# Optimization experiments

Hardware: AMD Instinct MI355X
Metric: run time of the kernel (lower is better)

Reference implementation:

```python
import jax, jax.numpy as jnp
import numpy as np

N = 50000          # nodes
E = 1250000        # edges (no self loops in raw data)
H = 2              # heads
C = 32             # out channels per head
DIN = 64           # dim_node
ED = 16            # edge_dim
G = 16             # graphs in batch
NC = 5             # num classes
SLOPE = 0.2        # GATConv leaky_relu negative_slope


def _glorot(key, shape):
    fan = shape[0] if len(shape) == 2 else shape[-1]
    return jax.random.normal(key, shape, jnp.float32) * (1.0 / np.sqrt(fan))


def setup_inputs() -> dict:
    key = jax.random.key(0)
    ks = jax.random.split(key, 24)
    x = jax.random.normal(ks[0], (N, DIN), jnp.float32)
    dst = jax.random.randint(ks[1], (E,), 0, N)
    off = jax.random.randint(ks[2], (E,), 1, N)
    src = (dst + off) % N  # guarantees src != dst (PyG removes self loops before re-adding)
    edge_index = jnp.stack([src, dst]).astype(jnp.int32)
    edge_attr = jax.random.normal(ks[3], (E, ED), jnp.float32)
    batch = jnp.sort(jax.random.randint(ks[4], (N,), 0, G)).astype(jnp.int32)
    inp = dict(x=x, edge_index=edge_index, edge_attr=edge_attr, batch=batch)
    # layer 1: in=DIN, heads=H, out=C, concat -> H*C
    inp["W1"] = _glorot(ks[5], (DIN, H * C)); inp["asrc1"] = _glorot(ks[6], (H, C))
    inp["adst1"] = _glorot(ks[7], (H, C)); inp["We1"] = _glorot(ks[8], (ED, H * C))
    inp["ae1"] = _glorot(ks[9], (H, C)); inp["b1"] = jnp.zeros((H * C,), jnp.float32)
    # layer 2: in=H*C, heads=H, out=C, concat
    inp["W2"] = _glorot(ks[10], (H * C, H * C)); inp["asrc2"] = _glorot(ks[11], (H, C))
    inp["adst2"] = _glorot(ks[12], (H, C)); inp["We2"] = _glorot(ks[13], (ED, H * C))
    inp["ae2"] = _glorot(ks[14], (H, C)); inp["b2"] = jnp.zeros((H * C,), jnp.float32)
    # layer 3: in=H*C, heads=1, out=C, concat=False
    inp["W3"] = _glorot(ks[15], (H * C, C)); inp["asrc3"] = _glorot(ks[16], (1, C))
    inp["adst3"] = _glorot(ks[17], (1, C)); inp["We3"] = _glorot(ks[18], (ED, C))
    inp["ae3"] = _glorot(ks[19], (1, C)); inp["b3"] = jnp.zeros((C,), jnp.float32)
    # ffn: Linear(C, NC) + softmax (dropout is identity in eval)
    inp["Wf"] = _glorot(ks[20], (C, NC)); inp["bf"] = jnp.zeros((NC,), jnp.float32)
    return inp


def _gat_layer(h_in, src, dst, eattr, W, asrc, adst, We, ae, b, heads, out, concat):
    n = h_in.shape[0]
    h = (h_in @ W).reshape(n, heads, out)                      # [N,H,C]
    s_src = jnp.einsum('nhc,hc->nh', h, asrc)                  # per-node src scores
    s_dst = jnp.einsum('nhc,hc->nh', h, adst)
    he = (eattr @ We).reshape(-1, heads, out)                  # [E,H,C]
    s_e = jnp.einsum('ehc,hc->eh', he, ae)
    logit = jax.nn.leaky_relu(s_src[src] + s_dst[dst] + s_e, SLOPE)  # [E,H]
    m = jax.ops.segment_max(logit, dst, num_segments=n)
    ex = jnp.exp(logit - m[dst])
    den = jax.ops.segment_sum(ex, dst, num_segments=n)
    alpha = ex / (den[dst] + 1e-16)                            # segment softmax per dst node
    agg = jax.ops.segment_sum(h[src] * alpha[..., None], dst, num_segments=n)  # [N,H,C]
    out_x = agg.reshape(n, heads * out) if concat else agg.mean(axis=1)
    return out_x + b


def _gat_forward(x, edge_index, edge_attr, batch,
                 W1, asrc1, adst1, We1, ae1, b1,
                 W2, asrc2, adst2, We2, ae2, b2,
                 W3, asrc3, adst3, We3, ae3, b3,
                 Wf, bf):
    src, dst = edge_index[0], edge_index[1]
    n = x.shape[0]
    # add_self_loops with fill_value='mean': self-loop edge_attr = mean of incoming edge_attr
    deg = jax.ops.segment_sum(jnp.ones((src.shape[0],), x.dtype), dst, num_segments=n)
    self_attr = jax.ops.segment_sum(edge_attr, dst, num_segments=n) / jnp.maximum(deg, 1.0)[:, None]
    loop = jnp.arange(n, dtype=src.dtype)
    src_a = jnp.concatenate([src, loop])
    dst_a = jnp.concatenate([dst, loop])
    eattr_a = jnp.concatenate([edge_attr, self_attr], axis=0)

    h = jax.nn.relu(_gat_layer(x, src_a, dst_a, eattr_a, W1, asrc1, adst1, We1, ae1, b1, H, C, True))
    h = jax.nn.relu(_gat_layer(h, src_a, dst_a, eattr_a, W2, asrc2, adst2, We2, ae2, b2, H, C, True))
    h = jax.nn.relu(_gat_layer(h, src_a, dst_a, eattr_a, W3, asrc3, adst3, We3, ae3, b3, 1, C, False))

    # global mean pool per graph
    cnt = jax.ops.segment_sum(jnp.ones((n,), h.dtype), batch, num_segments=G)
    pooled = jax.ops.segment_sum(h, batch, num_segments=G) / jnp.maximum(cnt, 1.0)[:, None]
    # ffn: Dropout (identity at eval) -> Linear -> Softmax(dim=1)
    return jax.nn.softmax(pooled @ Wf + bf, axis=1)


def reference(x, edge_index, edge_attr, batch,
              W1, asrc1, adst1, We1, ae1, b1,
              W2, asrc2, adst2, We2, ae2, b2,
              W3, asrc3, adst3, We3, ae3, b3,
              Wf, bf):
    return _gat_forward(x, edge_index, edge_attr, batch,
                        W1, asrc1, adst1, We1, ae1, b1,
                        W2, asrc2, adst2, We2, ae2, b2,
                        W3, asrc3, adst3, We3, ae3, b3,
                        Wf, bf)
```

## Files before the change

kernel.cpp:

```cpp
#include <hip/hip_runtime.h>
#include <math.h>

#define NN 50000
#define EE 1250000
#define GG 16
#define NCLS 5
#define NBIN 391
#define BINSHIFT 7
#define CAPB 3900

constexpr size_t AL(size_t x){ return (x + 255) & ~size_t(255); }
constexpr size_t OFF_DEG    = 0;
constexpr size_t OFF_ROWPTR = OFF_DEG + AL((size_t)NN*4);
constexpr size_t OFF_CURSOR = OFF_ROWPTR + AL((size_t)(NN+1)*4);
constexpr size_t OFF_SRCS   = OFF_CURSOR + AL((size_t)NN*4);
constexpr size_t OFF_SE12   = OFF_SRCS + AL((size_t)EE*2);
constexpr size_t OFF_SE34   = OFF_SE12 + AL((size_t)EE*4);
constexpr size_t OFF_SE5    = OFF_SE34 + AL((size_t)EE*4);
constexpr size_t OFF_SSRC   = OFF_SE5 + AL((size_t)EE*2);
constexpr size_t OFF_SDST   = OFF_SSRC + AL((size_t)NN*2*4);
constexpr size_t OFF_STAG   = OFF_SDST + AL((size_t)NN*2*4);
constexpr size_t OFF_BUFH   = OFF_STAG + AL((size_t)NBIN*CAPB*16);
constexpr size_t OFF_BUFO   = OFF_BUFH + AL((size_t)NN*32*4);
constexpr size_t OFF_WEFF   = OFF_BUFO + AL((size_t)NN*64*4);
constexpr size_t OFF_POOL   = OFF_WEFF + AL(80*4);

__device__ __forceinline__ float leaky(float x){ return x > 0.f ? x : 0.2f*x; }
__device__ __forceinline__ unsigned rne_bf16(float x){
    unsigned u = __float_as_uint(x);
    return (u + 0x7FFFu + ((u >> 16) & 1u)) >> 16;
}

__global__ void weff_kernel(const float* __restrict__ We1, const float* __restrict__ ae1,
                            const float* __restrict__ We2, const float* __restrict__ ae2,
                            const float* __restrict__ We3, const float* __restrict__ ae3,
                            float* __restrict__ weff){
    int t = threadIdx.x;
    if (t >= 80) return;
    int j = t >> 4, d = t & 15;
    const float* We; const float* ae; int hc, h;
    if (j == 0){ We = We1; ae = ae1; hc = 64; h = 0; }
    else if (j == 1){ We = We1; ae = ae1; hc = 64; h = 1; }
    else if (j == 2){ We = We2; ae = ae2; hc = 64; h = 0; }
    else if (j == 3){ We = We2; ae = ae2; hc = 64; h = 1; }
    else { We = We3; ae = ae3; hc = 32; h = 0; }
    float s = 0.f;
    for (int c = 0; c < 32; ++c) s += We[d*hc + h*32 + c] * ae[h*32 + c];
    weff[j*16 + d] = s;
}

__global__ void binit_kernel(int* __restrict__ bincursor){
    int b = blockIdx.x*256 + threadIdx.x;
    if (b < NBIN) bincursor[b] = b*CAPB;
}

__global__ void binA_kernel(const int* __restrict__ src, const int* __restrict__ dst,
                            const float* __restrict__ eattr, const float* __restrict__ weff,
                            int* __restrict__ bincursor, int4* __restrict__ staging, int nE){
    __shared__ int lcount[NBIN];
    __shared__ int lbase[NBIN];
    __shared__ float w[80];
    int tid = threadIdx.x;
    if (tid < 80) w[tid] = weff[tid];
    for (int i = tid; i < NBIN; i += 1024) lcount[i] = 0;
    __syncthreads();
    int base = blockIdx.x * 8192;
    int w0[8], bn[8], idx[8]; unsigned p01[8], p23[8], p4[8];
    #pragma unroll
    for (int k = 0; k < 8; ++k){
        int i = base + k*1024 + tid;
        if (i < nE){
            int d = dst[i];
            int s = src[i];
            bn[k]  = d >> BINSHIFT;
            w0[k]  = s | ((d & 127) << 16);
            const float4* row = (const float4*)(eattr + (size_t)i*16);
            float4 a0 = row[0], a1 = row[1], a2 = row[2], a3 = row[3];
            float a[16] = {a0.x,a0.y,a0.z,a0.w, a1.x,a1.y,a1.z,a1.w,
                           a2.x,a2.y,a2.z,a2.w, a3.x,a3.y,a3.z,a3.w};
            float sj[5];
            #pragma unroll
            for (int j = 0; j < 5; ++j){
                float s2 = 0.f;
                #pragma unroll
                for (int d2 = 0; d2 < 16; ++d2) s2 += a[d2]*w[j*16+d2];
                sj[j] = s2;
            }
            p01[k] = rne_bf16(sj[0]) | (rne_bf16(sj[1]) << 16);
            p23[k] = rne_bf16(sj[2]) | (rne_bf16(sj[3]) << 16);
            p4[k]  = rne_bf16(sj[4]);
            idx[k] = atomicAdd(&lcount[bn[k]], 1);
        } else bn[k] = -1;
    }
    __syncthreads();
    for (int i = tid; i < NBIN; i += 1024)
        lbase[i] = atomicAdd(&bincursor[i], lcount[i]);
    __syncthreads();
    #pragma unroll
    for (int k = 0; k < 8; ++k)
        if (bn[k] >= 0)
            staging[lbase[bn[k]] + idx[k]] = make_int4(w0[k], (int)p01[k], (int)p23[k], (int)p4[k]);
}

__global__ void hist_kernel(const int4* __restrict__ staging, const int* __restrict__ bincursor,
                            int* __restrict__ deg, int nN){
    __shared__ int lcnt[128];
    int b = blockIdx.x;
    int tid = threadIdx.x;
    if (tid < 128) lcnt[tid] = 0;
    __syncthreads();
    int base = b*CAPB;
    int cnt = bincursor[b] - base;
    for (int k = tid; k < cnt; k += 256)
        atomicAdd(&lcnt[staging[base + k].x >> 16], 1);
    __syncthreads();
    int lo = b << BINSHIFT;
    if (tid < 128 && lo + tid < nN) deg[lo + tid] = lcnt[tid];
}

__global__ void bsum_kernel(const int* __restrict__ deg, int* __restrict__ bsum, int nN){
    __shared__ int s[1024];
    int tid = threadIdx.x;
    int i = blockIdx.x*1024 + tid;
    s[tid] = (i < nN) ? deg[i] : 0;
    __syncthreads();
    for (int off = 512; off > 0; off >>= 1){
        if (tid < off) s[tid] += s[tid+off];
        __syncthreads();
    }
    if (tid == 0) bsum[blockIdx.x] = s[0];
}

__global__ void bscan_kernel(const int* __restrict__ bsum, int* __restrict__ boff,
                             int* __restrict__ rowptr, int nB, int nN){
    int lane = threadIdx.x;
    int v = (lane < nB) ? bsum[lane] : 0;
    int incl = v;
    #pragma unroll
    for (int off = 1; off < 64; off <<= 1){
        int t = __shfl_up(incl, off);
        if (lane >= off) incl += t;
    }
    if (lane < nB) boff[lane] = incl - v;
    if (lane == 63) rowptr[nN] = incl;
}

__global__ void wptr_kernel(const int* __restrict__ deg, const int* __restrict__ boff,
                            int* __restrict__ rowptr, int nN){
    __shared__ int s[1024];
    int tid = threadIdx.x;
    int i = blockIdx.x*1024 + tid;
    int v = (i < nN) ? deg[i] : 0;
    s[tid] = v;
    __syncthreads();
    for (int off = 1; off < 1024; off <<= 1){
        int t = (tid >= off) ? s[tid-off] : 0;
        __syncthreads();
        s[tid] += t;
        __syncthreads();
    }
    if (i < nN) rowptr[i] = boff[blockIdx.x] + s[tid] - v;
}

__global__ void binB_kernel(const int* __restrict__ rowptr, const int4* __restrict__ staging,
                            unsigned short* __restrict__ srcs, unsigned* __restrict__ se12,
                            unsigned* __restrict__ se34, unsigned short* __restrict__ se5, int nN){
    __shared__ int4 lout[CAPB];
    __shared__ int lcnt[128];
    int b = blockIdx.x;
    int lo = b << BINSHIFT;
    int hi = min(lo + 128, nN);
    int r0 = rowptr[lo], r1 = rowptr[hi];
    int cnt = r1 - r0;
    int sbase = b*CAPB;
    int tid = threadIdx.x;
    if (tid < 128) lcnt[tid] = 0;
    __syncthreads();
    for (int k = tid; k < cnt; k += 1024){
        int4 v = staging[sbase + k];
        int dl = v.x >> 16;
        int rank = atomicAdd(&lcnt[dl], 1);
        int target = rowptr[lo + dl] - r0 + rank;
        v.x &= 0xFFFF;
        if (target < CAPB) lout[target] = v;
        else {
            srcs[r0 + target] = (unsigned short)v.x;
            se12[r0 + target] = (unsigned)v.y;
            se34[r0 + target] = (unsigned)v.z;
            se5[r0 + target]  = (unsigned short)v.w;
        }
    }
    __syncthreads();
    int m = min(cnt, CAPB);
    for (int k = tid; k < m; k += 1024){
        int4 v = lout[k];
        srcs[r0 + k] = (unsigned short)v.x;
        se12[r0 + k] = (unsigned)v.y;
        se34[r0 + k] = (unsigned)v.z;
        se5[r0 + k]  = (unsigned short)v.w;
    }
}

template<int OUTC>
__global__ void transform_kernel(const float* __restrict__ in, const float* __restrict__ W,
                                 const float* __restrict__ asrc, const float* __restrict__ adst,
                                 unsigned* __restrict__ hout2, float* __restrict__ ssrc,
                                 float* __restrict__ sdst, int nN){
    constexpr int R = 256/OUTC;
    __shared__ float Ws[64*OUTC];
    __shared__ float ins[R*64];
    int tid = threadIdx.x;
    for (int i = tid; i < 64*OUTC; i += 256) Ws[i] = W[i];
    int base = blockIdx.x * R;
    for (int i = tid; i < R*64; i += 256){
        int n = base + i/64;
        ins[i] = (n < nN) ? in[(size_t)n*64 + (i & 63)] : 0.f;
    }
    __syncthreads();
    int r = tid / OUTC, c = tid % OUTC;
    int n = base + r;
    float acc = 0.f;
    #pragma unroll
    for (int d = 0; d < 64; ++d) acc += ins[r*64 + d] * Ws[d*OUTC + c];
    float ps = acc * asrc[c];
    float pd = acc * adst[c];
    #pragma unroll
    for (int m = 1; m <= 16; m <<= 1){ ps += __shfl_xor(ps, m); pd += __shfl_xor(pd, m); }
    float accN = __shfl_xor(acc, 1);
    if (n < nN){
        if ((c & 1) == 0){
            unsigned pk = rne_bf16(acc) | (rne_bf16(accN) << 16);
            hout2[(size_t)n*(OUTC/2) + (c >> 1)] = pk;
        }
        constexpr int HEADS = OUTC/32;
        if ((c & 31) == 0){
            int h = c >> 5;
            ssrc[n*HEADS + h] = ps;
            sdst[n*HEADS + h] = pd;
        }
    }
}

template<int OUTC>
__global__ void agg_kernel(const int* __restrict__ rowptr, const unsigned short* __restrict__ srcs,
                           const unsigned* __restrict__ sePa, const unsigned short* __restrict__ sePb,
                           const float* __restrict__ ssrc, const float* __restrict__ sdst,
                           const unsigned* __restrict__ hbuf2, const float* __restrict__ bias,
                           float* __restrict__ outbuf, int nN){
    constexpr int HEADS = OUTC/32;
    constexpr int HALF  = OUTC/4;
    constexpr int EPI   = 64/HALF;
    int wid = threadIdx.x >> 6;
    int lane = threadIdx.x & 63;
    int n = blockIdx.x*4 + wid;
    if (n >= nN) return;
    int row_start = rowptr[n], row_end = rowptr[n+1];
    int degn = row_end - row_start;
    float sd0 = sdst[n*HEADS + 0];
    float sd1 = (HEADS == 2) ? sdst[n*HEADS + 1] : 0.f;

    int sub = lane / HALF;
    int lc  = lane & (HALF - 1);
    int h   = (HEADS == 2) ? ((4*lc) >> 5) : 0;

    float acc0=0.f, acc1=0.f, acc2=0.f, acc3=0.f, den=0.f;
    float ssp0=0.f, ssp1=0.f;
    const uint2* hb2 = (const uint2*)hbuf2;

    for (int p0 = row_start; p0 < row_end; p0 += 64){
        int myp = p0 + lane;
        int srcreg = 0; unsigned wpk = 0; float w0s = 0.f;
        if (myp < row_end){
            srcreg = srcs[myp];
            if (HEADS == 2){
                unsigned pk = sePa[myp];
                float e0 = __uint_as_float(pk << 16);
                float e1 = __uint_as_float(pk & 0xFFFF0000u);
                ssp0 += e0; ssp1 += e1;
                float2 sv = ((const float2*)ssrc)[srcreg];
                float w0 = __expf(leaky(sv.x + sd0 + e0));
                float w1 = __expf(leaky(sv.y + sd1 + e1));
                wpk = rne_bf16(w0) | (rne_bf16(w1) << 16);
            } else {
                float e0 = __uint_as_float(((unsigned)sePb[myp]) << 16);
                ssp0 += e0;
                w0s = __expf(leaky(ssrc[srcreg] + sd0 + e0));
            }
        }
        int cnt = min(64, row_end - p0);
        for (int q = sub; q < cnt; q += EPI){
            int sj = __shfl(srcreg, q);
            float wj;
            if (HEADS == 2){
                unsigned wq = __shfl(wpk, q);
                wj = h ? __uint_as_float(wq & 0xFFFF0000u) : __uint_as_float(wq << 16);
            } else {
                wj = __shfl(w0s, q);
            }
            den += wj;
            uint2 hv = hb2[(size_t)sj*(OUTC/4) + lc];
            acc0 += wj * __uint_as_float(hv.x << 16);
            acc1 += wj * __uint_as_float(hv.x & 0xFFFF0000u);
            acc2 += wj * __uint_as_float(hv.y << 16);
            acc3 += wj * __uint_as_float(hv.y & 0xFFFF0000u);
        }
    }

    #pragma unroll
    for (int m = HALF; m < 64; m <<= 1){
        acc0 += __shfl_xor(acc0, m);
        acc1 += __shfl_xor(acc1, m);
        acc2 += __shfl_xor(acc2, m);
        acc3 += __shfl_xor(acc3, m);
        den  += __shfl_xor(den, m);
    }
    #pragma unroll
    for (int m = 1; m < 64; m <<= 1){
        ssp0 += __shfl_xor(ssp0, m);
        if (HEADS == 2) ssp1 += __shfl_xor(ssp1, m);
    }

    float invdeg = 1.f / (float)max(degn, 1);
    float srh = ssrc[n*HEADS + h];
    float sdh = h ? sd1 : sd0;
    float ssh = h ? ssp1 : ssp0;
    float wself = __expf(leaky(srh + sdh + ssh*invdeg));
    uint2 hv = hb2[(size_t)n*(OUTC/4) + lc];
    acc0 += wself * __uint_as_float(hv.x << 16);
    acc1 += wself * __uint_as_float(hv.x & 0xFFFF0000u);
    acc2 += wself * __uint_as_float(hv.y << 16);
    acc3 += wself * __uint_as_float(hv.y & 0xFFFF0000u);
    den += wself;

    if (lane < HALF){
        float inv = 1.f / (den + 1e-16f);
        float4 o;
        o.x = fmaxf(acc0*inv + bias[4*lc+0], 0.f);
        o.y = fmaxf(acc1*inv + bias[4*lc+1], 0.f);
        o.z = fmaxf(acc2*inv + bias[4*lc+2], 0.f);
        o.w = fmaxf(acc3*inv + bias[4*lc+3], 0.f);
        ((float4*)outbuf)[(size_t)n*(OUTC/4) + lc] = o;
    }
}

__global__ void pool_kernel(const float* __restrict__ h3, const int* __restrict__ batch,
                            float* __restrict__ pool, float* __restrict__ cnt, int nN){
    __shared__ float accs[GG*32];
    __shared__ float acccnt[GG];
    int tid = threadIdx.x;
    for (int i = tid; i < GG*32; i += 256) accs[i] = 0.f;
    if (tid < GG) acccnt[tid] = 0.f;
    __syncthreads();
    int r = tid >> 5, c = tid & 31;
    int base = blockIdx.x * 512;
    int end = min(base + 512, nN);
    for (int n = base + r; n < end; n += 8){
        int g = batch[n];
        atomicAdd(&accs[g*32 + c], h3[(size_t)n*32 + c]);
        if (c == 0) atomicAdd(&acccnt[g], 1.f);
    }
    __syncthreads();
    for (int i = tid; i < GG*32; i += 256) atomicAdd(&pool[i], accs[i]);
    if (tid < GG) atomicAdd(&cnt[tid], acccnt[tid]);
}

__global__ void final_kernel(const float* __restrict__ pool, const float* __restrict__ cnt,
                             const float* __restrict__ Wf, const float* __restrict__ bf,
                             float* __restrict__ out){
    int g = threadIdx.x;
    if (g >= GG) return;
    float ic = 1.f / fmaxf(cnt[g], 1.f);
    float lg[NCLS];
    #pragma unroll
    for (int k = 0; k < NCLS; ++k) lg[k] = bf[k];
    for (int c = 0; c < 32; ++c){
        float v = pool[g*32 + c] * ic;
        #pragma unroll
        for (int k = 0; k < NCLS; ++k) lg[k] += v * Wf[c*NCLS + k];
    }
    float mx = lg[0];
    #pragma unroll
    for (int k = 1; k < NCLS; ++k) mx = fmaxf(mx, lg[k]);
    float sum = 0.f, ex[NCLS];
    #pragma unroll
    for (int k = 0; k < NCLS; ++k){ ex[k] = expf(lg[k] - mx); sum += ex[k]; }
    #pragma unroll
    for (int k = 0; k < NCLS; ++k) out[g*NCLS + k] = ex[k]/sum;
}

extern "C" void kernel_launch(void* const* d_in, const int* in_sizes, int n_in,
                              void* d_out, int out_size, void* d_ws, size_t ws_size,
                              hipStream_t stream){
    const float* x     = (const float*)d_in[0];
    const int*   eidx  = (const int*)d_in[1];
    const float* eattr = (const float*)d_in[2];
    const int*   batch = (const int*)d_in[3];
    const float* W1 = (const float*)d_in[4];  const float* asrc1 = (const float*)d_in[5];
    const float* adst1 = (const float*)d_in[6]; const float* We1 = (const float*)d_in[7];
    const float* ae1 = (const float*)d_in[8];  const float* b1 = (const float*)d_in[9];
    const float* W2 = (const float*)d_in[10]; const float* asrc2 = (const float*)d_in[11];
    const float* adst2 = (const float*)d_in[12]; const float* We2 = (const float*)d_in[13];
    const float* ae2 = (const float*)d_in[14]; const float* b2 = (const float*)d_in[15];
    const float* W3 = (const float*)d_in[16]; const float* asrc3 = (const float*)d_in[17];
    const float* adst3 = (const float*)d_in[18]; const float* We3 = (const float*)d_in[19];
    const float* ae3 = (const float*)d_in[20]; const float* b3 = (const float*)d_in[21];
    const float* Wf = (const float*)d_in[22]; const float* bf = (const float*)d_in[23];
    float* out = (float*)d_out;

    char* ws = (char*)d_ws;
    int*   deg    = (int*)(ws + OFF_DEG);
    int*   rowptr = (int*)(ws + OFF_ROWPTR);
    int*   curs   = (int*)(ws + OFF_CURSOR);
    unsigned short* srcs = (unsigned short*)(ws + OFF_SRCS);
    unsigned* se12 = (unsigned*)(ws + OFF_SE12);
    unsigned* se34 = (unsigned*)(ws + OFF_SE34);
    unsigned short* se5 = (unsigned short*)(ws + OFF_SE5);
    float* ssrc   = (float*)(ws + OFF_SSRC);
    float* sdst   = (float*)(ws + OFF_SDST);
    int4*  staging = (int4*)(ws + OFF_STAG);
    unsigned* bufH = (unsigned*)(ws + OFF_BUFH);
    float* bufO   = (float*)(ws + OFF_BUFO);
    float* weff   = (float*)(ws + OFF_WEFF);
    float* pool   = (float*)(ws + OFF_POOL);
    float* cnt    = pool + GG*32;

    int* bincursor = curs;
    int* bsum      = curs + 512;
    int* boff      = curs + 1024;

    const int* srcA = eidx;
    const int* dstA = eidx + EE;

    hipMemsetAsync(pool, 0, (GG*32 + GG)*4, stream);

    weff_kernel<<<1, 128, 0, stream>>>(We1, ae1, We2, ae2, We3, ae3, weff);
    binit_kernel<<<(NBIN+255)/256, 256, 0, stream>>>(bincursor);
    binA_kernel<<<(EE + 8191)/8192, 1024, 0, stream>>>(srcA, dstA, eattr, weff, bincursor, staging, EE);
    hist_kernel<<<NBIN, 256, 0, stream>>>(staging, bincursor, deg, NN);
    int sgrid = (NN + 1023)/1024;
    bsum_kernel<<<sgrid, 1024, 0, stream>>>(deg, bsum, NN);
    bscan_kernel<<<1, 64, 0, stream>>>(bsum, boff, rowptr, sgrid, NN);
    wptr_kernel<<<sgrid, 1024, 0, stream>>>(deg, boff, rowptr, NN);
    binB_kernel<<<NBIN, 1024, 0, stream>>>(rowptr, staging, srcs, se12, se34, se5, NN);

    int ngrid4 = (NN + 3)/4;
    int ngrid8 = (NN + 7)/8;
    transform_kernel<64><<<ngrid4, 256, 0, stream>>>(x, W1, asrc1, adst1, bufH, ssrc, sdst, NN);
    agg_kernel<64><<<ngrid4, 256, 0, stream>>>(rowptr, srcs, se12, nullptr,
                                               ssrc, sdst, bufH, b1, bufO, NN);
    transform_kernel<64><<<ngrid4, 256, 0, stream>>>(bufO, W2, asrc2, adst2, bufH, ssrc, sdst, NN);
    agg_kernel<64><<<ngrid4, 256, 0, stream>>>(rowptr, srcs, se34, nullptr,
                                               ssrc, sdst, bufH, b2, bufO, NN);
    transform_kernel<32><<<ngrid8, 256, 0, stream>>>(bufO, W3, asrc3, adst3, bufH, ssrc, sdst, NN);
    agg_kernel<32><<<ngrid4, 256, 0, stream>>>(rowptr, srcs, nullptr, se5,
                                               ssrc, sdst, bufH, b3, bufO, NN);
    pool_kernel<<<(NN + 511)/512, 256, 0, stream>>>(bufO, batch, pool, cnt, NN);
    final_kernel<<<1, 64, 0, stream>>>(pool, cnt, Wf, bf, out);
}
```

Before: 274.4 us.

## Rework GAT aggregation lane mapping and shrink binA per-block edge count

The aggregation kernel now packs the source index and the bf16 attention weight into one word, so each gathered edge needs a single shuffle. For two-head layers each lane pair computes one head's weight per edge, so 32 edges are processed per chunk and each lane gathers only its own head's half-row. The edge-binning kernel handles 2048 edges per block instead of 8192, giving more blocks and fewer registers per thread at the cost of more global atomics on the bin cursors. Packing the source into 16 bits relies on node ids staying below 65536.

```diff
diff --git a/kernel.cpp b/kernel.cpp
--- a/kernel.cpp
+++ b/kernel.cpp
@@ -30,6 +30,8 @@
     unsigned u = __float_as_uint(x);
     return (u + 0x7FFFu + ((u >> 16) & 1u)) >> 16;
 }
+__device__ __forceinline__ float bf16lo(unsigned p){ return __uint_as_float(p << 16); }
+__device__ __forceinline__ float bf16hi(unsigned p){ return __uint_as_float(p & 0xFFFF0000u); }
 
 __global__ void weff_kernel(const float* __restrict__ We1, const float* __restrict__ ae1,
                             const float* __restrict__ We2, const float* __restrict__ ae2,
@@ -64,10 +66,10 @@
     if (tid < 80) w[tid] = weff[tid];
     for (int i = tid; i < NBIN; i += 1024) lcount[i] = 0;
     __syncthreads();
-    int base = blockIdx.x * 8192;
-    int w0[8], bn[8], idx[8]; unsigned p01[8], p23[8], p4[8];
-    #pragma unroll
-    for (int k = 0; k < 8; ++k){
+    int base = blockIdx.x * 2048;
+    int w0[2], bn[2], idx[2]; unsigned p01[2], p23[2], p4[2];
+    #pragma unroll
+    for (int k = 0; k < 2; ++k){
         int i = base + k*1024 + tid;
         if (i < nE){
             int d = dst[i];
@@ -97,7 +99,7 @@
         lbase[i] = atomicAdd(&bincursor[i], lcount[i]);
     __syncthreads();
     #pragma unroll
-    for (int k = 0; k < 8; ++k)
+    for (int k = 0; k < 2; ++k)
         if (bn[k] >= 0)
             staging[lbase[bn[k]] + idx[k]] = make_int4(w0[k], (int)p01[k], (int)p23[k], (int)p4[k]);
 }
@@ -248,8 +250,6 @@
                            const unsigned* __restrict__ hbuf2, const float* __restrict__ bias,
                            float* __restrict__ outbuf, int nN){
     constexpr int HEADS = OUTC/32;
-    constexpr int HALF  = OUTC/4;
-    constexpr int EPI   = 64/HALF;
     int wid = threadIdx.x >> 6;
     int lane = threadIdx.x & 63;
     int n = blockIdx.x*4 + wid;
@@ -259,87 +259,118 @@
     float sd0 = sdst[n*HEADS + 0];
     float sd1 = (HEADS == 2) ? sdst[n*HEADS + 1] : 0.f;
 
-    int sub = lane / HALF;
-    int lc  = lane & (HALF - 1);
-    int h   = (HEADS == 2) ? ((4*lc) >> 5) : 0;
-
-    float acc0=0.f, acc1=0.f, acc2=0.f, acc3=0.f, den=0.f;
-    float ssp0=0.f, ssp1=0.f;
     const uint2* hb2 = (const uint2*)hbuf2;
-
-    for (int p0 = row_start; p0 < row_end; p0 += 64){
-        int myp = p0 + lane;
-        int srcreg = 0; unsigned wpk = 0; float w0s = 0.f;
-        if (myp < row_end){
-            srcreg = srcs[myp];
-            if (HEADS == 2){
+    float acc0=0.f, acc1=0.f, acc2=0.f, acc3=0.f, den=0.f, sspL=0.f;
+
+    int h, lc;
+    if (HEADS == 2){ int s = lane >> 3; h = s & 1; lc = lane & 7; }
+    else           { h = 0; lc = lane & 7; }
+
+    if (HEADS == 2){
+        int eoff = lane >> 1, hp = lane & 1;
+        int q0 = (lane >> 4);
+        float sdh_p = hp ? sd1 : sd0;
+        for (int p0 = row_start; p0 < row_end; p0 += 32){
+            int myp = p0 + eoff;
+            unsigned wpk = 0;
+            if (myp < row_end){
+                int srcreg = srcs[myp];
                 unsigned pk = sePa[myp];
-                float e0 = __uint_as_float(pk << 16);
-                float e1 = __uint_as_float(pk & 0xFFFF0000u);
-                ssp0 += e0; ssp1 += e1;
-                float2 sv = ((const float2*)ssrc)[srcreg];
-                float w0 = __expf(leaky(sv.x + sd0 + e0));
-                float w1 = __expf(leaky(sv.y + sd1 + e1));
-                wpk = rne_bf16(w0) | (rne_bf16(w1) << 16);
-            } else {
-                float e0 = __uint_as_float(((unsigned)sePb[myp]) << 16);
-                ssp0 += e0;
-                w0s = __expf(leaky(ssrc[srcreg] + sd0 + e0));
+                float e = hp ? bf16hi(pk) : bf16lo(pk);
+                sspL += e;
+                float sh = ssrc[2*srcreg + hp];
+                float wv = __expf(leaky(sh + sdh_p + e));
+                wpk = (unsigned)srcreg | (rne_bf16(wv) << 16);
             }
-        }
-        int cnt = min(64, row_end - p0);
-        for (int q = sub; q < cnt; q += EPI){
-            int sj = __shfl(srcreg, q);
-            float wj;
-            if (HEADS == 2){
-                unsigned wq = __shfl(wpk, q);
-                wj = h ? __uint_as_float(wq & 0xFFFF0000u) : __uint_as_float(wq << 16);
-            } else {
-                wj = __shfl(w0s, q);
+            int cnt = min(32, row_end - p0);
+            for (int qq = q0; qq < cnt; qq += 4){
+                unsigned u = __shfl(wpk, 2*qq + h);
+                int sj = u & 0xFFFF;
+                float wj = __uint_as_float(u & 0xFFFF0000u);
+                den += wj;
+                uint2 hv = hb2[(size_t)sj*16 + h*8 + lc];
+                acc0 += wj * bf16lo(hv.x);
+                acc1 += wj * bf16hi(hv.x);
+                acc2 += wj * bf16lo(hv.y);
+                acc3 += wj * bf16hi(hv.y);
             }
-            den += wj;
-            uint2 hv = hb2[(size_t)sj*(OUTC/4) + lc];
-            acc0 += wj * __uint_as_float(hv.x << 16);
-            acc1 += wj * __uint_as_float(hv.x & 0xFFFF0000u);
-            acc2 += wj * __uint_as_float(hv.y << 16);
-            acc3 += wj * __uint_as_float(hv.y & 0xFFFF0000u);
-        }
-    }
-
-    #pragma unroll
-    for (int m = HALF; m < 64; m <<= 1){
-        acc0 += __shfl_xor(acc0, m);
-        acc1 += __shfl_xor(acc1, m);
-        acc2 += __shfl_xor(acc2, m);
-        acc3 += __shfl_xor(acc3, m);
-        den  += __shfl_xor(den, m);
-    }
-    #pragma unroll
-    for (int m = 1; m < 64; m <<= 1){
-        ssp0 += __shfl_xor(ssp0, m);
-        if (HEADS == 2) ssp1 += __shfl_xor(ssp1, m);
-    }
-
-    float invdeg = 1.f / (float)max(degn, 1);
-    float srh = ssrc[n*HEADS + h];
-    float sdh = h ? sd1 : sd0;
-    float ssh = h ? ssp1 : ssp0;
-    float wself = __expf(leaky(srh + sdh + ssh*invdeg));
-    uint2 hv = hb2[(size_t)n*(OUTC/4) + lc];
-    acc0 += wself * __uint_as_float(hv.x << 16);
-    acc1 += wself * __uint_as_float(hv.x & 0xFFFF0000u);
-    acc2 += wself * __uint_as_float(hv.y << 16);
-    acc3 += wself * __uint_as_float(hv.y & 0xFFFF0000u);
-    den += wself;
-
-    if (lane < HALF){
-        float inv = 1.f / (den + 1e-16f);
-        float4 o;
-        o.x = fmaxf(acc0*inv + bias[4*lc+0], 0.f);
-        o.y = fmaxf(acc1*inv + bias[4*lc+1], 0.f);
-        o.z = fmaxf(acc2*inv + bias[4*lc+2], 0.f);
-        o.w = fmaxf(acc3*inv + bias[4*lc+3], 0.f);
-        ((float4*)outbuf)[(size_t)n*(OUTC/4) + lc] = o;
+        }
+        #pragma unroll
+        for (int m = 2; m < 64; m <<= 1) sspL += __shfl_xor(sspL, m);
+        float ssh = __shfl(sspL, h);
+        #pragma unroll
+        for (int m = 16; m < 64; m <<= 1){
+            acc0 += __shfl_xor(acc0, m); acc1 += __shfl_xor(acc1, m);
+            acc2 += __shfl_xor(acc2, m); acc3 += __shfl_xor(acc3, m);
+            den  += __shfl_xor(den, m);
+        }
+        float invdeg = 1.f / (float)max(degn, 1);
+        float srh = ssrc[2*n + h];
+        float sdh = h ? sd1 : sd0;
+        float wself = __expf(leaky(srh + sdh + ssh*invdeg));
+        uint2 hv = hb2[(size_t)n*16 + h*8 + lc];
+        acc0 += wself * bf16lo(hv.x); acc1 += wself * bf16hi(hv.x);
+        acc2 += wself * bf16lo(hv.y); acc3 += wself * bf16hi(hv.y);
+        den += wself;
+        if (lane < 16){
+            float inv = 1.f / (den + 1e-16f);
+            int idx4 = h*8 + lc;
+            float4 o;
+            o.x = fmaxf(acc0*inv + bias[4*idx4+0], 0.f);
+            o.y = fmaxf(acc1*inv + bias[4*idx4+1], 0.f);
+            o.z = fmaxf(acc2*inv + bias[4*idx4+2], 0.f);
+            o.w = fmaxf(acc3*inv + bias[4*idx4+3], 0.f);
+            ((float4*)outbuf)[(size_t)n*16 + idx4] = o;
+        }
+    } else {
+        int q0 = lane >> 3;
+        for (int p0 = row_start; p0 < row_end; p0 += 64){
+            int myp = p0 + lane;
+            unsigned wpk = 0;
+            if (myp < row_end){
+                int srcreg = srcs[myp];
+                float e = __uint_as_float(((unsigned)sePb[myp]) << 16);
+                sspL += e;
+                float wv = __expf(leaky(ssrc[srcreg] + sd0 + e));
+                wpk = (unsigned)srcreg | (rne_bf16(wv) << 16);
+            }
+            int cnt = min(64, row_end - p0);
+            for (int qq = q0; qq < cnt; qq += 8){
+                unsigned u = __shfl(wpk, qq);
+                int sj = u & 0xFFFF;
+                float wj = __uint_as_float(u & 0xFFFF0000u);
+                den += wj;
+                uint2 hv = hb2[(size_t)sj*8 + lc];
+                acc0 += wj * bf16lo(hv.x);
+                acc1 += wj * bf16hi(hv.x);
+                acc2 += wj * bf16lo(hv.y);
+                acc3 += wj * bf16hi(hv.y);
+            }
+        }
+        #pragma unroll
+        for (int m = 1; m < 64; m <<= 1) sspL += __shfl_xor(sspL, m);
+        float ssh = sspL;
+        #pragma unroll
+        for (int m = 8; m < 64; m <<= 1){
+            acc0 += __shfl_xor(acc0, m); acc1 += __shfl_xor(acc1, m);
+            acc2 += __shfl_xor(acc2, m); acc3 += __shfl_xor(acc3, m);
+            den  += __shfl_xor(den, m);
+        }
+        float invdeg = 1.f / (float)max(degn, 1);
+        float wself = __expf(leaky(ssrc[n] + sd0 + ssh*invdeg));
+        uint2 hv = hb2[(size_t)n*8 + lc];
+        acc0 += wself * bf16lo(hv.x); acc1 += wself * bf16hi(hv.x);
+        acc2 += wself * bf16lo(hv.y); acc3 += wself * bf16hi(hv.y);
+        den += wself;
+        if (lane < 8){
+            float inv = 1.f / (den + 1e-16f);
+            float4 o;
+            o.x = fmaxf(acc0*inv + bias[4*lc+0], 0.f);
+            o.y = fmaxf(acc1*inv + bias[4*lc+1], 0.f);
+            o.z = fmaxf(acc2*inv + bias[4*lc+2], 0.f);
+            o.w = fmaxf(acc3*inv + bias[4*lc+3], 0.f);
+            ((float4*)outbuf)[(size_t)n*8 + lc] = o;
+        }
     }
 }
 
@@ -435,7 +466,7 @@
 
     weff_kernel<<<1, 128, 0, stream>>>(We1, ae1, We2, ae2, We3, ae3, weff);
     binit_kernel<<<(NBIN+255)/256, 256, 0, stream>>>(bincursor);
-    binA_kernel<<<(EE + 8191)/8192, 1024, 0, stream>>>(srcA, dstA, eattr, weff, bincursor, staging, EE);
+    binA_kernel<<<(EE + 2047)/2048, 1024, 0, stream>>>(srcA, dstA, eattr, weff, bincursor, staging, EE);
     hist_kernel<<<NBIN, 256, 0, stream>>>(staging, bincursor, deg, NN);
     int sgrid = (NN + 1023)/1024;
     bsum_kernel<<<sgrid, 1024, 0, stream>>>(deg, bsum, NN);
```

Result: no change. 275.8 us (+0.5%).
